# Performance work log

Hardware: AMD Instinct MI355X
Metric: run time of the kernel (lower is better)

The kernel has to match this reference:

```python
import jax, jax.numpy as jnp
import numpy as np

HIDDEN = 1024
HEADS = 16
HEAD_DIM = HIDDEN // HEADS
BS, SEQ = 4, 2048
NEG = -1.0e9


def setup_inputs() -> dict:
    key = jax.random.key(0)
    ks = jax.random.split(key, 10)
    s = 1.0 / np.sqrt(HIDDEN)
    inp = {
        "hidden_states": jax.random.normal(ks[0], (BS, SEQ, HIDDEN), jnp.float32),
        # causal mask: 1 at masked (future) positions, broadcast over [bs,h,s,s]
        "causal_mask": jnp.triu(jnp.ones((SEQ, SEQ), jnp.bool_), k=1),
        # padding mask: 1 at padded key positions; last 128 tokens of each row padded
        "padding_mask": jnp.arange(SEQ)[None, :] >= (SEQ - 128),
        "q_w": jax.random.normal(ks[1], (HIDDEN, HIDDEN), jnp.float32) * s,
        "q_b": jnp.zeros((HIDDEN,), jnp.float32),
        "k_w": jax.random.normal(ks[2], (HIDDEN, HIDDEN), jnp.float32) * s,
        "k_b": jnp.zeros((HIDDEN,), jnp.float32),
        "v_w": jax.random.normal(ks[3], (HIDDEN, HIDDEN), jnp.float32) * s,
        "v_b": jnp.zeros((HIDDEN,), jnp.float32),
        "o_w": jax.random.normal(ks[4], (HIDDEN, HIDDEN), jnp.float32) * s,
        "o_b": jnp.zeros((HIDDEN,), jnp.float32),
    }
    inp["padding_mask"] = jnp.broadcast_to(inp["padding_mask"], (BS, SEQ))
    return inp


def reference(hidden_states, causal_mask, padding_mask,
              q_w, q_b, k_w, k_b, v_w, v_b, o_w, o_b):
    bs, seq, _ = hidden_states.shape
    # projections (torch Linear: x @ W.T + b)
    def proj(w, b):
        y = jnp.einsum("bsh,oh->bso", hidden_states, w) + b
        return y.reshape(bs, seq, HEADS, HEAD_DIM).transpose(0, 2, 1, 3)  # [b,h,s,d]

    q = proj(q_w, q_b)
    k = proj(k_w, k_b)
    v = proj(v_w, v_b)

    scores = jnp.einsum("bhqd,bhkd->bhqk", q, k) / np.sqrt(HEAD_DIM)  # [b,h,s,s]
    scores = scores + causal_mask.astype(scores.dtype) * NEG
    scores = scores + padding_mask[:, None, None, :].astype(scores.dtype) * NEG
    weights = jax.nn.softmax(scores, axis=-1)
    # dropout p=0.0 -> identity
    out = jnp.einsum("bhqk,bhkd->bhqd", weights, v)
    out = out.transpose(0, 2, 1, 3).reshape(bs, seq, HIDDEN)
    out = jnp.einsum("bsh,oh->bso", out, o_w) + o_b
    return out
```

## Files before the change

### kernel.cpp

```cpp
#include <hip/hip_runtime.h>
#include <hip/hip_bf16.h>

#define HIDDEN 1024
#define HEADS  16
#define HDIM   64
#define BSZ    4
#define SEQ    2048
#define MROWS  (BSZ * SEQ)
#define KPAD   1920
#define EXPC   0.1803368801111204f

typedef unsigned short ushort_t;
typedef __attribute__((ext_vector_type(8))) short short8;
typedef __attribute__((ext_vector_type(4))) short short4v;
typedef __attribute__((ext_vector_type(4))) float floatx4;

__device__ __forceinline__ ushort_t f2bf(float f) {
    union { float f; unsigned u; } v; v.f = f;
    return (ushort_t)((v.u + 0x7fffu + ((v.u >> 16) & 1u)) >> 16);
}

__device__ __forceinline__ void g2l16(const ushort_t* g, ushort_t* l) {
    __builtin_amdgcn_global_load_lds(
        (const __attribute__((address_space(1))) void*)g,
        (__attribute__((address_space(3))) void*)l,
        16, 0, 0);
}

__device__ __forceinline__ short4v pk4(float4 v) {
    union { __hip_bfloat162 h; unsigned u; } c0, c1;
    float2 t0; t0.x = v.x; t0.y = v.y; c0.h = __float22bfloat162_rn(t0);
    float2 t1; t1.x = v.z; t1.y = v.w; c1.h = __float22bfloat162_rn(t1);
    short4v o;
    o[0] = (short)(c0.u & 0xffff); o[1] = (short)(c0.u >> 16);
    o[2] = (short)(c1.u & 0xffff); o[3] = (short)(c1.u >> 16);
    return o;
}

__global__ void cvt_in(const float* __restrict__ x,
                       const float* __restrict__ wq,
                       const float* __restrict__ wk,
                       const float* __restrict__ wv,
                       ushort_t* __restrict__ dst)
{
    const size_t i4 = ((size_t)blockIdx.x * 256 + threadIdx.x) * 4;
    const float* s; size_t off;
    if (i4 < 8388608)       { s = x;  off = i4; }
    else if (i4 < 9437184)  { s = wq; off = i4 - 8388608; }
    else if (i4 < 10485760) { s = wk; off = i4 - 9437184; }
    else                    { s = wv; off = i4 - 10485760; }
    *(short4v*)(dst + i4) = pk4(*(const float4*)(s + off));
}

__global__ void cvt_w(const float* __restrict__ w, ushort_t* __restrict__ dst)
{
    const size_t i4 = ((size_t)blockIdx.x * 256 + threadIdx.x) * 4;
    *(short4v*)(dst + i4) = pk4(*(const float4*)(w + i4));
}

template <int MODE>
__global__ void gemm_bt(const ushort_t* __restrict__ A,
                        const ushort_t* __restrict__ W0,
                        const ushort_t* __restrict__ W1,
                        const ushort_t* __restrict__ W2,
                        const float* __restrict__ B0,
                        const float* __restrict__ B1,
                        const float* __restrict__ B2,
                        ushort_t* __restrict__ Oq,
                        ushort_t* __restrict__ Ok,
                        ushort_t* __restrict__ Ovt,
                        float* __restrict__ Cf)
{
    __shared__ __align__(16) ushort_t sA[128 * 32];
    __shared__ __align__(16) ushort_t sB[128 * 32];

    const int t = threadIdx.x;
    const int w = t >> 6, l = t & 63;
    const int m0 = blockIdx.y * 128;
    const int n0g = blockIdx.x * 128;

    const int which = (MODE == 0) ? (n0g >> 10) : 0;
    const ushort_t* W  = (MODE == 0) ? (which == 0 ? W0 : which == 1 ? W1 : W2) : W0;
    const float*    Bv = (MODE == 0) ? (which == 0 ? B0 : which == 1 ? B1 : B2) : B0;
    const int n0 = (MODE == 0) ? (n0g & 1023) : n0g;

    const int wy = w >> 1, wx = w & 1;
    floatx4 acc[4][4] = {};

    const int srow = t >> 2;
    const int sk8  = (t & 3) * 8;
    const ushort_t* Ag = A + (size_t)(m0 + srow) * 1024 + sk8;
    const ushort_t* Wg = W + (size_t)(n0 + srow) * 1024 + sk8;
    ushort_t* lA = &sA[t * 8];
    ushort_t* lB = &sB[t * 8];

    const int fr  = l & 15;
    const int fq8 = (l >> 4) * 8;

    for (int kb = 0; kb < 32; ++kb) {
        __syncthreads();
        const int kk = kb * 32;
        g2l16(Ag + kk,         lA);
        g2l16(Ag + kk + 65536, lA + 2048);
        g2l16(Wg + kk,         lB);
        g2l16(Wg + kk + 65536, lB + 2048);
        __syncthreads();

        short8 af[4], bfrg[4];
#pragma unroll
        for (int mi = 0; mi < 4; ++mi)
            af[mi] = *(const short8*)&sA[(wy * 64 + mi * 16 + fr) * 32 + fq8];
#pragma unroll
        for (int ni = 0; ni < 4; ++ni)
            bfrg[ni] = *(const short8*)&sB[(wx * 64 + ni * 16 + fr) * 32 + fq8];
#pragma unroll
        for (int mi = 0; mi < 4; ++mi)
#pragma unroll
            for (int ni = 0; ni < 4; ++ni)
                acc[mi][ni] = __builtin_amdgcn_mfma_f32_16x16x32_bf16(
                    af[mi], bfrg[ni], acc[mi][ni], 0, 0, 0);
    }

    const int rq = (l >> 4) * 4;
    if (MODE == 1) {
#pragma unroll
        for (int ni = 0; ni < 4; ++ni) {
            const int n = n0 + wx * 64 + ni * 16 + fr;
            const float bias = Bv[n];
#pragma unroll
            for (int mi = 0; mi < 4; ++mi) {
                const int mrow = m0 + wy * 64 + mi * 16 + rq;
#pragma unroll
                for (int r = 0; r < 4; ++r)
                    Cf[(size_t)(mrow + r) * 1024 + n] = acc[mi][ni][r] + bias;
            }
        }
    } else if (which == 2) {
#pragma unroll
        for (int ni = 0; ni < 4; ++ni) {
            const int n = n0 + wx * 64 + ni * 16 + fr;
            const float bias = Bv[n];
            const int h = n >> 6, d = n & 63;
#pragma unroll
            for (int mi = 0; mi < 4; ++mi) {
                const int mrow = m0 + wy * 64 + mi * 16 + rq;
                const int b = mrow >> 11, s0 = mrow & 2047;
                short4v pk;
#pragma unroll
                for (int r = 0; r < 4; ++r)
                    pk[r] = (short)f2bf(acc[mi][ni][r] + bias);
                *(short4v*)&Ovt[(((size_t)(b * 16 + h) * 64 + d) << 11) + s0] = pk;
            }
        }
    } else {
        ushort_t* Ot = which == 0 ? Oq : Ok;
        const float sc = (which == 0) ? EXPC : 1.0f;
#pragma unroll
        for (int ni = 0; ni < 4; ++ni) {
            const int n = n0 + wx * 64 + ni * 16 + fr;
            const float bias = Bv[n];
            const int h = n >> 6, d = n & 63;
#pragma unroll
            for (int mi = 0; mi < 4; ++mi) {
                const int mrow = m0 + wy * 64 + mi * 16 + rq;
#pragma unroll
                for (int r = 0; r < 4; ++r) {
                    const int m = mrow + r;
                    const int b = m >> 11, s = m & 2047;
                    Ot[(((size_t)(b * 16 + h) * SEQ + s) << 6) + d] =
                        f2bf((acc[mi][ni][r] + bias) * sc);
                }
            }
        }
    }
}

#define PSTR 76

__global__ __launch_bounds__(256, 2)
void attn_kernel(const ushort_t* __restrict__ Q,
                 const ushort_t* __restrict__ K,
                 const ushort_t* __restrict__ VT,
                 ushort_t* __restrict__ O)
{
    __shared__ __align__(16) ushort_t sK[2][64 * 72];
    __shared__ __align__(16) ushort_t sVT[2][64 * 72];
    __shared__ __align__(16) ushort_t sP[4][64 * PSTR];

    const int t = threadIdx.x;
    const int w = t >> 6, l = t & 63;
    const int lid = blockIdx.x;
    const int qt = (lid < 256) ? (lid >> 6) : (11 - (lid >> 6));
    const int hb = lid & 63;
    const int qs = qt << 8;
    const size_t headbase = (size_t)hb << 17;
    const int b = hb >> 4, h = hb & 15;

    const int f    = l & 15;
    const int g    = l >> 4;
    const int g8   = g * 8;
    const int row4 = g * 4;

    short8 qf[4][2];
#pragma unroll
    for (int m = 0; m < 4; ++m) {
        const ushort_t* gq = Q + headbase + ((size_t)(qs + w * 64 + m * 16 + f) << 6);
        qf[m][0] = *(const short8*)(gq + g8);
        qf[m][1] = *(const short8*)(gq + 32 + g8);
    }

    floatx4 accO[4][4] = {};
    float   psum[4] = {0.f, 0.f, 0.f, 0.f};

    const int mykb  = qt * 4 + w;
    const int kbmax = (qt * 4 + 3 < 29) ? qt * 4 + 3 : 29;

    const int srow = t >> 2, sc0 = (t & 3) * 16;
    const ushort_t* gkb = K  + headbase + (size_t)srow * 64 + sc0;
    const ushort_t* gvb = VT + headbase + ((size_t)srow << 11) + sc0;

    {
        const short8 k0 = *(const short8*)gkb;
        const short8 k1 = *(const short8*)(gkb + 8);
        const short8 v0 = *(const short8*)gvb;
        const short8 v1 = *(const short8*)(gvb + 8);
        *(short8*)&sK[0][srow * 72 + sc0]      = k0;
        *(short8*)&sK[0][srow * 72 + sc0 + 8]  = k1;
        *(short8*)&sVT[0][srow * 72 + sc0]     = v0;
        *(short8*)&sVT[0][srow * 72 + sc0 + 8] = v1;
    }

    for (int kb = 0; kb <= kbmax; ++kb) {
        __syncthreads();
        const int cur = kb & 1;
        const bool more = (kb < kbmax);

        short8 nk0, nk1, nv0, nv1;
        if (more) {
            const ushort_t* gk = gkb + (size_t)(kb + 1) * 4096;
            nk0 = *(const short8*)gk;
            nk1 = *(const short8*)(gk + 8);
            const ushort_t* gv = gvb + ((kb + 1) << 6);
            nv0 = *(const short8*)gv;
            nv1 = *(const short8*)(gv + 8);
        }

        if (kb <= mykb) {
            const bool diag = (kb == mykb);

            short8 kf[4][2], vf[4][2];
#pragma unroll
            for (int jt = 0; jt < 4; ++jt) {
                kf[jt][0] = *(const short8*)&sK[cur][(jt * 16 + f) * 72 + g8];
                kf[jt][1] = *(const short8*)&sK[cur][(jt * 16 + f) * 72 + 32 + g8];
            }
#pragma unroll
            for (int dj = 0; dj < 4; ++dj) {
                vf[dj][0] = *(const short8*)&sVT[cur][(dj * 16 + f) * 72 + g8];
                vf[dj][1] = *(const short8*)&sVT[cur][(dj * 16 + f) * 72 + 32 + g8];
            }

#pragma unroll
            for (int m = 0; m < 4; ++m) {
                floatx4 st4[4] = {};
#pragma unroll
                for (int jt = 0; jt < 4; ++jt) {
                    st4[jt] = __builtin_amdgcn_mfma_f32_16x16x32_bf16(kf[jt][0], qf[m][0], st4[jt], 0, 0, 0);
                    st4[jt] = __builtin_amdgcn_mfma_f32_16x16x32_bf16(kf[jt][1], qf[m][1], st4[jt], 0, 0, 0);
                }
                float lsum = 0.f;
#pragma unroll
                for (int jt = 0; jt < 4; ++jt) {
                    float pv[4];
#pragma unroll
                    for (int r = 0; r < 4; ++r)
                        pv[r] = __builtin_amdgcn_exp2f(st4[jt][r]);
                    if (diag) {
                        const int kloc = jt * 16 + row4;
                        const int qloc = m * 16 + f;
#pragma unroll
                        for (int r = 0; r < 4; ++r)
                            if (kloc + r > qloc) pv[r] = 0.f;
                    }
                    lsum += (pv[0] + pv[1]) + (pv[2] + pv[3]);
                    union { __hip_bfloat162 hh; unsigned u; } d01, d23;
                    float2 f0; f0.x = pv[0]; f0.y = pv[1]; d01.hh = __float22bfloat162_rn(f0);
                    float2 f1; f1.x = pv[2]; f1.y = pv[3]; d23.hh = __float22bfloat162_rn(f1);
                    short4v pk;
                    pk[0] = (short)(d01.u & 0xffff); pk[1] = (short)(d01.u >> 16);
                    pk[2] = (short)(d23.u & 0xffff); pk[3] = (short)(d23.u >> 16);
                    *(short4v*)&sP[w][(m * 16 + f) * PSTR + jt * 16 + row4] = pk;
                }
                psum[m] += lsum;
            }

            __asm__ volatile("s_waitcnt lgkmcnt(0)" ::: "memory");

#pragma unroll
            for (int m = 0; m < 4; ++m) {
                short8 pf0 = *(const short8*)&sP[w][(m * 16 + f) * PSTR + g8];
                short8 pf1 = *(const short8*)&sP[w][(m * 16 + f) * PSTR + 32 + g8];
#pragma unroll
                for (int dj = 0; dj < 4; ++dj) {
                    accO[m][dj] = __builtin_amdgcn_mfma_f32_16x16x32_bf16(pf0, vf[dj][0], accO[m][dj], 0, 0, 0);
                    accO[m][dj] = __builtin_amdgcn_mfma_f32_16x16x32_bf16(pf1, vf[dj][1], accO[m][dj], 0, 0, 0);
                }
            }
        }

        if (more) {
            const int nxt = cur ^ 1;
            *(short8*)&sK[nxt][srow * 72 + sc0]      = nk0;
            *(short8*)&sK[nxt][srow * 72 + sc0 + 8]  = nk1;
            *(short8*)&sVT[nxt][srow * 72 + sc0]     = nv0;
            *(short8*)&sVT[nxt][srow * 72 + sc0 + 8] = nv1;
        }
    }

    float rin[4];
#pragma unroll
    for (int m = 0; m < 4; ++m) {
        float ps = psum[m];
        ps += __shfl_xor(ps, 16);
        ps += __shfl_xor(ps, 32);
        rin[m] = 1.f / ps;
    }
    float rv[4][4];
#pragma unroll
    for (int m = 0; m < 4; ++m)
#pragma unroll
        for (int r = 0; r < 4; ++r)
            rv[m][r] = __shfl(rin[m], (l & 48) + row4 + r);

#pragma unroll
    for (int m = 0; m < 4; ++m)
#pragma unroll
        for (int dj = 0; dj < 4; ++dj)
#pragma unroll
            for (int r = 0; r < 4; ++r) {
                const int qg = qs + w * 64 + m * 16 + row4 + r;
                O[(size_t)(b * SEQ + qg) * 1024 + h * 64 + dj * 16 + f] =
                    f2bf(accO[m][dj][r] * rv[m][r]);
            }
}

extern "C" void kernel_launch(void* const* d_in, const int* in_sizes, int n_in,
                              void* d_out, int out_size, void* d_ws, size_t ws_size,
                              hipStream_t stream)
{
    const float* x     = (const float*)d_in[0];
    const float* qw    = (const float*)d_in[3];
    const float* qbias = (const float*)d_in[4];
    const float* kw    = (const float*)d_in[5];
    const float* kbias = (const float*)d_in[6];
    const float* vw    = (const float*)d_in[7];
    const float* vbias = (const float*)d_in[8];
    const float* ow    = (const float*)d_in[9];
    const float* obias = (const float*)d_in[10];
    float* out = (float*)d_out;

    ushort_t* Qws  = (ushort_t*)d_ws;
    ushort_t* Kws  = Qws + (size_t)MROWS * 1024;
    ushort_t* VTws = Kws + (size_t)MROWS * 1024;
    ushort_t* Ows  = VTws + (size_t)MROWS * 1024;

    ushort_t* xb  = (ushort_t*)d_out;
    ushort_t* qwb = xb + 8388608;
    ushort_t* kwb = xb + 9437184;
    ushort_t* vwb = xb + 10485760;
    ushort_t* owb = VTws;

    cvt_in<<<dim3(11264), 256, 0, stream>>>(x, qw, kw, vw, xb);

    gemm_bt<0><<<dim3(24, 64), 256, 0, stream>>>(
        xb, qwb, kwb, vwb, qbias, kbias, vbias, Qws, Kws, VTws, nullptr);

    attn_kernel<<<dim3(512), 256, 0, stream>>>(Qws, Kws, VTws, Ows);

    cvt_w<<<dim3(1024), 256, 0, stream>>>(ow, owb);

    gemm_bt<1><<<dim3(8, 64), 256, 0, stream>>>(
        Ows, owb, nullptr, nullptr, obias, nullptr, nullptr,
        nullptr, nullptr, nullptr, out);
}
```

Measured before the change: 272.2 us.

## Double GEMM K-tile to 64 and XOR-swizzle LDS layout in gemm_bt

The projection GEMM now stages a 64-wide K slice per iteration instead of 32, halving the loop trip count and the number of __syncthreads barriers. The global-to-LDS load mapping is rearranged so that each row's 16-byte chunks are XOR-swizzled by row index, and the MFMA fragment reads apply the same swizzle to avoid LDS bank conflicts. LDS use per block doubles, which may reduce occupancy.

Result: faster. 262.8 us (-3.5%).

```diff
diff --git a/kernel.cpp b/kernel.cpp
--- a/kernel.cpp
+++ b/kernel.cpp
@@ -71,8 +71,8 @@
                         ushort_t* __restrict__ Ovt,
                         float* __restrict__ Cf)
 {
-    __shared__ __align__(16) ushort_t sA[128 * 32];
-    __shared__ __align__(16) ushort_t sB[128 * 32];
+    __shared__ __align__(16) ushort_t sA[128 * 64];
+    __shared__ __align__(16) ushort_t sB[128 * 64];
 
     const int t = threadIdx.x;
     const int w = t >> 6, l = t & 63;
@@ -87,38 +87,46 @@
     const int wy = w >> 1, wx = w & 1;
     floatx4 acc[4][4] = {};
 
-    const int srow = t >> 2;
-    const int sk8  = (t & 3) * 8;
-    const ushort_t* Ag = A + (size_t)(m0 + srow) * 1024 + sk8;
-    const ushort_t* Wg = W + (size_t)(n0 + srow) * 1024 + sk8;
-    ushort_t* lA = &sA[t * 8];
-    ushort_t* lB = &sB[t * 8];
-
-    const int fr  = l & 15;
-    const int fq8 = (l >> 4) * 8;
-
-    for (int kb = 0; kb < 32; ++kb) {
+    const int srow0 = w * 32 + (l >> 3);
+    const int scc   = (((l & 7) ^ ((l >> 3) & 7)) << 3);
+    const ushort_t* Ag = A + (size_t)(m0 + srow0) * 1024 + scc;
+    const ushort_t* Wg = W + (size_t)(n0 + srow0) * 1024 + scc;
+    ushort_t* lA = &sA[(w * 2048) + l * 8];
+    ushort_t* lB = &sB[(w * 2048) + l * 8];
+
+    const int fr = l & 15;
+    const int g  = l >> 4;
+
+    for (int kb = 0; kb < 16; ++kb) {
         __syncthreads();
-        const int kk = kb * 32;
-        g2l16(Ag + kk,         lA);
-        g2l16(Ag + kk + 65536, lA + 2048);
-        g2l16(Wg + kk,         lB);
-        g2l16(Wg + kk + 65536, lB + 2048);
+        const int kk = kb * 64;
+#pragma unroll
+        for (int i = 0; i < 4; ++i) {
+            g2l16(Ag + kk + (size_t)i * 8192, lA + i * 512);
+            g2l16(Wg + kk + (size_t)i * 8192, lB + i * 512);
+        }
         __syncthreads();
 
-        short8 af[4], bfrg[4];
-#pragma unroll
-        for (int mi = 0; mi < 4; ++mi)
-            af[mi] = *(const short8*)&sA[(wy * 64 + mi * 16 + fr) * 32 + fq8];
-#pragma unroll
-        for (int ni = 0; ni < 4; ++ni)
-            bfrg[ni] = *(const short8*)&sB[(wx * 64 + ni * 16 + fr) * 32 + fq8];
-#pragma unroll
-        for (int mi = 0; mi < 4; ++mi)
-#pragma unroll
-            for (int ni = 0; ni < 4; ++ni)
-                acc[mi][ni] = __builtin_amdgcn_mfma_f32_16x16x32_bf16(
-                    af[mi], bfrg[ni], acc[mi][ni], 0, 0, 0);
+#pragma unroll
+        for (int ks = 0; ks < 2; ++ks) {
+            short8 af[4], bfrg[4];
+#pragma unroll
+            for (int mi = 0; mi < 4; ++mi) {
+                const int rA = wy * 64 + mi * 16 + fr;
+                af[mi] = *(const short8*)&sA[rA * 64 + ((((ks << 2) + g) ^ (rA & 7)) << 3)];
+            }
+#pragma unroll
+            for (int ni = 0; ni < 4; ++ni) {
+                const int rB = wx * 64 + ni * 16 + fr;
+                bfrg[ni] = *(const short8*)&sB[rB * 64 + ((((ks << 2) + g) ^ (rB & 7)) << 3)];
+            }
+#pragma unroll
+            for (int mi = 0; mi < 4; ++mi)
+#pragma unroll
+                for (int ni = 0; ni < 4; ++ni)
+                    acc[mi][ni] = __builtin_amdgcn_mfma_f32_16x16x32_bf16(
+                        af[mi], bfrg[ni], acc[mi][ni], 0, 0, 0);
+        }
     }
 
     const int rq = (l >> 4) * 4;
```
